# Performance work log

Measured on AMD Instinct MI355X. Metric: run time of the kernel, lower is better.

Reference implementation:

```python
import jax, jax.numpy as jnp
import numpy as np

B, LP, LQ, H = 16, 512, 512, 768


def setup_inputs() -> dict:
    key = jax.random.key(0)
    k0, k1, k2, k3 = jax.random.split(key, 4)
    proj_p = jax.random.normal(k0, (B, LP, H), dtype=jnp.float32)
    proj_q = jax.random.normal(k1, (B, LQ, H), dtype=jnp.float32)
    seq_len = jax.random.randint(k2, (B,), 1, LQ + 1)  # valid lengths in [1, LQ]
    W_trans = jax.random.normal(k3, (H, H), dtype=jnp.float32) / jnp.sqrt(H).astype(jnp.float32)
    b_trans = jnp.zeros((H,), dtype=jnp.float32)
    return {"proj_p": proj_p, "proj_q": proj_q, "seq_len": seq_len,
            "W_trans": W_trans, "b_trans": b_trans}


def reference(proj_p, proj_q, seq_len, W_trans, b_trans):
    # trans_q = trans_linear(proj_q): [B, Lq, H]
    trans_q = jnp.einsum('bqh,oh->bqo', proj_q, W_trans) + b_trans
    # attention scores: [B, Lp, Lq]
    att = jnp.einsum('bph,bqh->bpq', proj_p, trans_q)
    # masked_softmax (MedLane style): softmax(scores * mask), re-mask, renormalize
    mask = (jnp.arange(LQ)[None, None, :] < seq_len[:, None, None]).astype(att.dtype)
    probs = jax.nn.softmax(att * mask, axis=-1) * mask
    probs = probs / (jnp.sum(probs, axis=-1, keepdims=True) + 1e-13)
    # weighted sum of proj_q: [B, Lp, H]
    att_vec = jnp.einsum('bpq,bqh->bph', probs, proj_q)
    # output = ReLU(trans_linear(att_vec))
    out = jax.nn.relu(jnp.einsum('bph,oh->bpo', att_vec, W_trans) + b_trans)
    return out
```

## Files before the change

### kernel.cpp

```cpp
#include <hip/hip_runtime.h>

typedef _Float16 f16x8 __attribute__((ext_vector_type(8)));
typedef __attribute__((ext_vector_type(4))) float f32x4;
typedef unsigned short u16;

__device__ __forceinline__ u16 f2h(float f) {
    _Float16 h = (_Float16)f;
    return __builtin_bit_cast(u16, h);
}

#define GLDS(G, LBYTE)                                                         \
    __builtin_amdgcn_global_load_lds(                                          \
        (const __attribute__((address_space(1))) void*)(G),                    \
        (__attribute__((address_space(3))) void*)((char*)lds + (LBYTE)),       \
        16, 0, 0)

template<int OUT, bool BIAS, bool RELU, bool RS, bool TW, int GX, int GY>
__global__ __launch_bounds__(256, 3)
void gemm_nt(const u16* __restrict__ A, const u16* __restrict__ B,
             const float* __restrict__ bias, const float* __restrict__ rs,
             void* __restrict__ Cv, u16* __restrict__ CT,
             int K, int lda, int ldb, int ldc,
             long sA, long sB, long sC)
{
    __shared__ u16 lds[24576];
    constexpr int BOF  = 8192;
    constexpr int BUFB = 24576;
    constexpr int BUFE = 12288;

    const unsigned flat = blockIdx.x;
    const unsigned cpx  = gridDim.x >> 3;
    const unsigned id   = (flat & 7u) * cpx + (flat >> 3);
    const int bz  = (int)(id / (unsigned)(GX * GY));
    const int rem = (int)(id - (unsigned)bz * (GX * GY));
    const int by  = rem / GX;
    const int bx  = rem - by * GX;

    const int tid  = threadIdx.x;
    const int lane = tid & 63;
    const int wid  = tid >> 6;
    const int m0 = by * 128;
    const int n0 = bx * 64;

    const int rowS = tid >> 3;
    const int sl   = (tid & 7) ^ (rowS & 7);
    const unsigned ldsW = (unsigned)wid * 1024u;

    const u16* aS = A + (size_t)bz * sA + ((size_t)m0 + rowS) * lda + sl * 8;
    const u16* bS = B + (size_t)bz * sB + ((size_t)n0 + rowS) * ldb + sl * 8;

    const int wm = (wid & 1) * 64;
    const int wn = (wid >> 1) * 32;
    const int fr = lane & 15;
    const int fq = lane >> 4;

    f32x4 acc[4][2] = {};

    auto stage = [&](int bb, int k0) {
        GLDS(aS + k0,            bb +     0 + ldsW);
        GLDS(aS + k0 + 32 * lda, bb +  4096 + ldsW);
        GLDS(aS + k0 + 64 * lda, bb +  8192 + ldsW);
        GLDS(aS + k0 + 96 * lda, bb + 12288 + ldsW);
        GLDS(bS + k0,            bb + 16384 + ldsW);
        GLDS(bS + k0 + 32 * ldb, bb + 20480 + ldsW);
    };

    auto compute = [&](int be) {
#pragma unroll
        for (int w = 0; w < 2; ++w) {
            const int sw = (((w << 2) | fq) ^ (fr & 7)) << 3;
            f16x8 vah[4], vbh[2];
#pragma unroll
            for (int i = 0; i < 4; ++i)
                vah[i] = *(const f16x8*)(lds + be + (wm + i * 16 + fr) * 64 + sw);
#pragma unroll
            for (int j = 0; j < 2; ++j)
                vbh[j] = *(const f16x8*)(lds + be + BOF + (wn + j * 16 + fr) * 64 + sw);
#pragma unroll
            for (int i = 0; i < 4; ++i)
#pragma unroll
                for (int j = 0; j < 2; ++j)
                    acc[i][j] = __builtin_amdgcn_mfma_f32_16x16x32_f16(vah[i], vbh[j], acc[i][j], 0, 0, 0);
        }
    };

    stage(0, 0);
    __syncthreads();
    for (int k0 = 0; k0 < K; k0 += 128) {
        if (k0 + 64 < K) stage(BUFB, k0 + 64);
        compute(0);
        __syncthreads();
        if (k0 + 128 < K) stage(0, k0 + 128);
        compute(BUFE);
        __syncthreads();
    }

    float bj[2];
    if (BIAS) {
#pragma unroll
        for (int j = 0; j < 2; ++j) bj[j] = bias[n0 + wn + j * 16 + fr];
    }
    const long crow0 = m0 + wm + fq * 4;
    const long ccol0 = n0 + wn + fr;
    float* Cf = (float*)Cv + (size_t)bz * sC;
    u16*   Ch = (u16*)Cv   + (size_t)bz * sC;
    const float* rsb = RS ? (rs + (size_t)bz * 512) : nullptr;
    const int  bzT = (int)(crow0 >> 9);
    const long qb  = crow0 & 511;
#pragma unroll
    for (int i = 0; i < 4; ++i) {
        float rsv[4];
        if (RS) {
#pragma unroll
            for (int r = 0; r < 4; ++r) rsv[r] = 1.0f - rsb[crow0 + i * 16 + r];
        }
#pragma unroll
        for (int j = 0; j < 2; ++j) {
            ushort4 tw;
#pragma unroll
            for (int r = 0; r < 4; ++r) {
                float v = acc[i][j][r];
                if (BIAS) v += RS ? bj[j] * rsv[r] : bj[j];
                if (RELU) v = fmaxf(v, 0.0f);
                const size_t idx = (size_t)(crow0 + i * 16 + r) * ldc + ccol0 + j * 16;
                if (OUT == 0) Cf[idx] = v;
                else {
                    const u16 h = f2h(v);
                    Ch[idx] = h;
                    if (TW) (&tw.x)[r] = h;
                }
            }
            if (OUT == 1 && TW) {
                *(ushort4*)(CT + (size_t)bzT * 768 * 512
                               + (size_t)(ccol0 + j * 16) * 512 + qb + i * 16) = tw;
            }
        }
    }
}

__global__ __launch_bounds__(256)
void cvt_all(const float* __restrict__ x0, u16* __restrict__ y0,
             const float* __restrict__ x1, u16* __restrict__ y1, int n4,
             const float* __restrict__ xw, u16* __restrict__ yw, int nW4)
{
    int i = blockIdx.x * 256 + threadIdx.x;
    const int stride = gridDim.x * 256;
    for (; i < n4; i += stride) {
        float4 v0 = ((const float4*)x0)[i];
        float4 v1 = ((const float4*)x1)[i];
        ushort4 h0, h1;
        h0.x = f2h(v0.x); h0.y = f2h(v0.y); h0.z = f2h(v0.z); h0.w = f2h(v0.w);
        h1.x = f2h(v1.x); h1.y = f2h(v1.y); h1.z = f2h(v1.z); h1.w = f2h(v1.w);
        ((ushort4*)y0)[i] = h0;
        ((ushort4*)y1)[i] = h1;
        if (i < nW4) {
            float4 vw = ((const float4*)xw)[i];
            ushort4 hw;
            hw.x = f2h(vw.x); hw.y = f2h(vw.y); hw.z = f2h(vw.z); hw.w = f2h(vw.w);
            ((ushort4*)yw)[i] = hw;
        }
    }
}

__global__ __launch_bounds__(256)
void softmax_kernel(float* __restrict__ att, const int* __restrict__ seq_len,
                    float* __restrict__ rsout)
{
    const int row = blockIdx.x;
    const int b   = row >> 9;
    float* s = att + (size_t)row * 512;
    const int L = seq_len[b];
    const int tid = threadIdx.x;

    __shared__ float red[4];

    const float v0 = s[tid];
    const float v1 = s[tid + 256];
    const bool  k0 = (tid < L);
    const bool  k1 = (tid + 256 < L);
    const float s0 = k0 ? v0 : 0.0f;
    const float s1 = k1 ? v1 : 0.0f;

    float m = fmaxf(s0, s1);
#pragma unroll
    for (int o = 32; o > 0; o >>= 1) m = fmaxf(m, __shfl_down(m, o));
    if ((tid & 63) == 0) red[tid >> 6] = m;
    __syncthreads();
    const float M = fmaxf(fmaxf(red[0], red[1]), fmaxf(red[2], red[3]));
    __syncthreads();

    const float e0 = k0 ? expf(s0 - M) : 0.0f;
    const float e1 = k1 ? expf(s1 - M) : 0.0f;

    float zs = e0 + e1;
#pragma unroll
    for (int o = 32; o > 0; o >>= 1) zs += __shfl_down(zs, o);
    if ((tid & 63) == 0) red[tid >> 6] = zs;
    __syncthreads();
    const float sve = red[0] + red[1] + red[2] + red[3];

    const float Z   = sve + (float)(512 - L) * expf(-M);
    const float S   = sve / Z;
    const float inv = 1.0f / (S + 1e-13f);
    const float sc  = inv / Z;

    u16* o16 = (u16*)s;
    o16[tid]       = f2h(k0 ? e0 * sc : 0.0f);
    o16[tid + 256] = f2h(k1 ? e1 * sc : 0.0f);
    if (tid == 0) rsout[row] = S * inv;
}

extern "C" void kernel_launch(void* const* d_in, const int* in_sizes, int n_in,
                              void* d_out, int out_size, void* d_ws, size_t ws_size,
                              hipStream_t stream)
{
    (void)in_sizes; (void)n_in; (void)out_size; (void)ws_size;
    constexpr int B = 16, L = 512, H = 768;
    constexpr size_t NPQ = (size_t)B * L * H;
    constexpr size_t NW  = (size_t)H * H;

    const float* proj_p  = (const float*)d_in[0];
    const float* proj_q  = (const float*)d_in[1];
    const int*   seq_len = (const int*)d_in[2];
    const float* W       = (const float*)d_in[3];
    const float* bias    = (const float*)d_in[4];
    float* out = (float*)d_out;

    u16* ws   = (u16*)d_ws;
    u16* pq16 = ws;
    u16* pp16 = pq16 + NPQ;
    u16* W16  = pp16 + NPQ;
    u16* tqT  = W16 + NW;
    float* att = (float*)(tqT + NPQ);
    float* rs  = att + (size_t)B * L * L;

    u16* tq16 = (u16*)d_out;

    cvt_all<<<2048, 256, 0, stream>>>(proj_q, pq16, proj_p, pp16, (int)(NPQ / 4),
                                      W, W16, (int)(NW / 4));

    gemm_nt<1, true, false, false, true, 12, 64><<<768, 256, 0, stream>>>(
        pq16, W16, bias, nullptr, tq16, tqT, H, H, H, H, 0, 0, 0);

    gemm_nt<0, false, false, false, false, 8, 4><<<512, 256, 0, stream>>>(
        pp16, tq16, nullptr, nullptr, att, nullptr, H, H, H, L,
        (long)L * H, (long)L * H, (long)L * L);

    softmax_kernel<<<B * L, 256, 0, stream>>>(att, seq_len, rs);

    gemm_nt<0, true, true, true, false, 12, 4><<<768, 256, 0, stream>>>(
        (const u16*)att, tqT, bias, rs, out, nullptr,
        L, 1024, L, H, (long)L * 1024, (long)H * L, (long)L * H);
}
```

Baseline: 71.47 us.

## Fuse fp32-to-fp16 conversion into GEMM loads and drop the convert kernel

Removes the separate cvt_all pass. The GEMMs now read fp32 proj_q, proj_p and W directly, convert them in registers and write fp16 tiles to LDS. This removes one kernel launch and a full write and reread of the fp16 copies. The staging path moves from direct global-to-LDS async loads to register-staged loads with explicit LDS stores and lgkmcnt barriers, which adds register pressure and VALU conversion work inside the GEMM main loop. It also repeats the conversion for each tile that re-reads the same data, and the fp32 reads double the global bytes per tile.

```diff
diff --git a/kernel.cpp b/kernel.cpp
--- a/kernel.cpp
+++ b/kernel.cpp
@@ -9,15 +9,23 @@
     return __builtin_bit_cast(u16, h);
 }
 
-#define GLDS(G, LBYTE)                                                         \
-    __builtin_amdgcn_global_load_lds(                                          \
-        (const __attribute__((address_space(1))) void*)(G),                    \
-        (__attribute__((address_space(3))) void*)((char*)lds + (LBYTE)),       \
-        16, 0, 0)
-
-template<int OUT, bool BIAS, bool RELU, bool RS, bool TW, int GX, int GY>
+__device__ __forceinline__ f16x8 cvt8(float4 a, float4 b) {
+    f16x8 r;
+    r[0] = (_Float16)a.x; r[1] = (_Float16)a.y; r[2] = (_Float16)a.z; r[3] = (_Float16)a.w;
+    r[4] = (_Float16)b.x; r[5] = (_Float16)b.y; r[6] = (_Float16)b.z; r[7] = (_Float16)b.w;
+    return r;
+}
+
+#define LGKM0_BAR()                                                            \
+    do {                                                                       \
+        asm volatile("s_waitcnt lgkmcnt(0)" ::: "memory");                     \
+        __builtin_amdgcn_s_barrier();                                          \
+    } while (0)
+
+template<bool AF32, bool BF32, int OUT, bool BIAS, bool RELU, bool RS, bool TW,
+         int GX, int GY>
 __global__ __launch_bounds__(256, 3)
-void gemm_nt(const u16* __restrict__ A, const u16* __restrict__ B,
+void gemm_nt(const void* __restrict__ Av, const void* __restrict__ Bv,
              const float* __restrict__ bias, const float* __restrict__ rs,
              void* __restrict__ Cv, u16* __restrict__ CT,
              int K, int lda, int ldb, int ldc,
@@ -25,7 +33,6 @@
 {
     __shared__ u16 lds[24576];
     constexpr int BOF  = 8192;
-    constexpr int BUFB = 24576;
     constexpr int BUFE = 12288;
 
     const unsigned flat = blockIdx.x;
@@ -43,11 +50,19 @@
     const int n0 = bx * 64;
 
     const int rowS = tid >> 3;
-    const int sl   = (tid & 7) ^ (rowS & 7);
-    const unsigned ldsW = (unsigned)wid * 1024u;
-
-    const u16* aS = A + (size_t)bz * sA + ((size_t)m0 + rowS) * lda + sl * 8;
-    const u16* bS = B + (size_t)bz * sB + ((size_t)n0 + rowS) * ldb + sl * 8;
+    const int cg   = tid & 7;
+    const int slw  = cg ^ (rowS & 7);
+
+    const float* aF = nullptr; const u16* aH = nullptr;
+    const float* bF = nullptr; const u16* bH = nullptr;
+    if constexpr (AF32)
+        aF = (const float*)Av + (size_t)bz * sA + ((size_t)(m0 + rowS)) * lda + cg * 8;
+    else
+        aH = (const u16*)Av + (size_t)bz * sA + ((size_t)(m0 + rowS)) * lda + cg * 8;
+    if constexpr (BF32)
+        bF = (const float*)Bv + (size_t)bz * sB + ((size_t)(n0 + rowS)) * ldb + cg * 8;
+    else
+        bH = (const u16*)Bv + (size_t)bz * sB + ((size_t)(n0 + rowS)) * ldb + cg * 8;
 
     const int wm = (wid & 1) * 64;
     const int wn = (wid >> 1) * 32;
@@ -56,13 +71,51 @@
 
     f32x4 acc[4][2] = {};
 
-    auto stage = [&](int bb, int k0) {
-        GLDS(aS + k0,            bb +     0 + ldsW);
-        GLDS(aS + k0 + 32 * lda, bb +  4096 + ldsW);
-        GLDS(aS + k0 + 64 * lda, bb +  8192 + ldsW);
-        GLDS(aS + k0 + 96 * lda, bb + 12288 + ldsW);
-        GLDS(bS + k0,            bb + 16384 + ldsW);
-        GLDS(bS + k0 + 32 * ldb, bb + 20480 + ldsW);
+    float4 rA[8]; f16x8 hA[4];
+    float4 rB[4]; f16x8 hB[2];
+
+    auto loadT = [&](int k0) {
+        if constexpr (AF32) {
+#pragma unroll
+            for (int c = 0; c < 4; ++c) {
+                const float* p = aF + (size_t)(c * 32) * lda + k0;
+                rA[2 * c]     = *(const float4*)p;
+                rA[2 * c + 1] = *(const float4*)(p + 4);
+            }
+        } else {
+#pragma unroll
+            for (int c = 0; c < 4; ++c)
+                hA[c] = *(const f16x8*)(aH + (size_t)(c * 32) * lda + k0);
+        }
+        if constexpr (BF32) {
+#pragma unroll
+            for (int c = 0; c < 2; ++c) {
+                const float* p = bF + (size_t)(c * 32) * ldb + k0;
+                rB[2 * c]     = *(const float4*)p;
+                rB[2 * c + 1] = *(const float4*)(p + 4);
+            }
+        } else {
+#pragma unroll
+            for (int c = 0; c < 2; ++c)
+                hB[c] = *(const f16x8*)(bH + (size_t)(c * 32) * ldb + k0);
+        }
+    };
+
+    auto writeT = [&](int be) {
+#pragma unroll
+        for (int c = 0; c < 4; ++c) {
+            f16x8 v;
+            if constexpr (AF32) v = cvt8(rA[2 * c], rA[2 * c + 1]);
+            else                v = hA[c];
+            *(f16x8*)(lds + be + (c * 32 + rowS) * 64 + slw * 8) = v;
+        }
+#pragma unroll
+        for (int c = 0; c < 2; ++c) {
+            f16x8 v;
+            if constexpr (BF32) v = cvt8(rB[2 * c], rB[2 * c + 1]);
+            else                v = hB[c];
+            *(f16x8*)(lds + be + BOF + (c * 32 + rowS) * 64 + slw * 8) = v;
+        }
     };
 
     auto compute = [&](int be) {
@@ -84,15 +137,21 @@
         }
     };
 
-    stage(0, 0);
-    __syncthreads();
+    loadT(0);
+    writeT(0);
+    loadT(64);
+    LGKM0_BAR();
     for (int k0 = 0; k0 < K; k0 += 128) {
-        if (k0 + 64 < K) stage(BUFB, k0 + 64);
         compute(0);
-        __syncthreads();
-        if (k0 + 128 < K) stage(0, k0 + 128);
+        writeT(BUFE);
+        if (k0 + 128 < K) loadT(k0 + 128);
+        LGKM0_BAR();
         compute(BUFE);
-        __syncthreads();
+        if (k0 + 128 < K) {
+            writeT(0);
+            if (k0 + 192 < K) loadT(k0 + 192);
+        }
+        LGKM0_BAR();
     }
 
     float bj[2];
@@ -139,30 +198,6 @@
 }
 
 __global__ __launch_bounds__(256)
-void cvt_all(const float* __restrict__ x0, u16* __restrict__ y0,
-             const float* __restrict__ x1, u16* __restrict__ y1, int n4,
-             const float* __restrict__ xw, u16* __restrict__ yw, int nW4)
-{
-    int i = blockIdx.x * 256 + threadIdx.x;
-    const int stride = gridDim.x * 256;
-    for (; i < n4; i += stride) {
-        float4 v0 = ((const float4*)x0)[i];
-        float4 v1 = ((const float4*)x1)[i];
-        ushort4 h0, h1;
-        h0.x = f2h(v0.x); h0.y = f2h(v0.y); h0.z = f2h(v0.z); h0.w = f2h(v0.w);
-        h1.x = f2h(v1.x); h1.y = f2h(v1.y); h1.z = f2h(v1.z); h1.w = f2h(v1.w);
-        ((ushort4*)y0)[i] = h0;
-        ((ushort4*)y1)[i] = h1;
-        if (i < nW4) {
-            float4 vw = ((const float4*)xw)[i];
-            ushort4 hw;
-            hw.x = f2h(vw.x); hw.y = f2h(vw.y); hw.z = f2h(vw.z); hw.w = f2h(vw.w);
-            ((ushort4*)yw)[i] = hw;
-        }
-    }
-}
-
-__global__ __launch_bounds__(256)
 void softmax_kernel(float* __restrict__ att, const int* __restrict__ seq_len,
                     float* __restrict__ rsout)
 {
@@ -217,7 +252,6 @@
     (void)in_sizes; (void)n_in; (void)out_size; (void)ws_size;
     constexpr int B = 16, L = 512, H = 768;
     constexpr size_t NPQ = (size_t)B * L * H;
-    constexpr size_t NW  = (size_t)H * H;
 
     const float* proj_p  = (const float*)d_in[0];
     const float* proj_q  = (const float*)d_in[1];
@@ -227,28 +261,22 @@
     float* out = (float*)d_out;
 
     u16* ws   = (u16*)d_ws;
-    u16* pq16 = ws;
-    u16* pp16 = pq16 + NPQ;
-    u16* W16  = pp16 + NPQ;
-    u16* tqT  = W16 + NW;
+    u16* tqT  = ws;
     float* att = (float*)(tqT + NPQ);
     float* rs  = att + (size_t)B * L * L;
 
     u16* tq16 = (u16*)d_out;
 
-    cvt_all<<<2048, 256, 0, stream>>>(proj_q, pq16, proj_p, pp16, (int)(NPQ / 4),
-                                      W, W16, (int)(NW / 4));
-
-    gemm_nt<1, true, false, false, true, 12, 64><<<768, 256, 0, stream>>>(
-        pq16, W16, bias, nullptr, tq16, tqT, H, H, H, H, 0, 0, 0);
-
-    gemm_nt<0, false, false, false, false, 8, 4><<<512, 256, 0, stream>>>(
-        pp16, tq16, nullptr, nullptr, att, nullptr, H, H, H, L,
+    gemm_nt<true, true, 1, true, false, false, true, 12, 64><<<768, 256, 0, stream>>>(
+        proj_q, W, bias, nullptr, tq16, tqT, H, H, H, H, 0, 0, 0);
+
+    gemm_nt<true, false, 0, false, false, false, false, 8, 4><<<512, 256, 0, stream>>>(
+        proj_p, tq16, nullptr, nullptr, att, nullptr, H, H, H, L,
         (long)L * H, (long)L * H, (long)L * L);
 
     softmax_kernel<<<B * L, 256, 0, stream>>>(att, seq_len, rs);
 
-    gemm_nt<0, true, true, true, false, 12, 4><<<768, 256, 0, stream>>>(
+    gemm_nt<false, false, 0, true, true, true, false, 12, 4><<<768, 256, 0, stream>>>(
         (const u16*)att, tqT, bias, rs, out, nullptr,
         L, 1024, L, H, (long)L * 1024, (long)H * L, (long)L * H);
 }
```

Measured after the change: 68.30 us (median of 2 runs). -4.4%, faster.
